# Optimization experiments

Hardware: AMD Instinct MI355X
Metric: run time of the kernel (lower is better)

The kernel has to match this reference:

```python
import jax, jax.numpy as jnp
import numpy as np
import math

B, N, D_POINTS, D_MODEL, K = 4, 4096, 512, 256, 16


def _gather(points, idx):
    # points: [B, N, C], idx: [B, S, K] -> [B, S, K, C]
    return jax.vmap(lambda p, i: p[i])(points, idx)


def setup_inputs() -> dict:
    key = jax.random.key(0)
    ks = jax.random.split(key, 20)
    def lin(k_, fan_in, fan_out):
        lim = 1.0 / math.sqrt(fan_in)
        return jax.random.uniform(k_, (fan_in, fan_out), jnp.float32, -lim, lim)
    inp = {
        "xyz": jax.random.normal(ks[0], (B, N, 3), jnp.float32),
        "features": jax.random.normal(ks[1], (B, N, D_POINTS), jnp.float32),
        # fc1: d_points -> d_model
        "W1": lin(ks[2], D_POINTS, D_MODEL), "b1": jnp.zeros((D_MODEL,), jnp.float32),
        # fc2: d_model -> d_points
        "W2": lin(ks[3], D_MODEL, D_POINTS), "b2": jnp.zeros((D_POINTS,), jnp.float32),
        # fc_delta: 3 -> d_model -> d_model
        "Wd1": lin(ks[4], 3, D_MODEL), "bd1": jnp.zeros((D_MODEL,), jnp.float32),
        "Wd2": lin(ks[5], D_MODEL, D_MODEL), "bd2": jnp.zeros((D_MODEL,), jnp.float32),
        # fc_gamma: d_model -> d_model -> d_model
        "Wg1": lin(ks[6], D_MODEL, D_MODEL), "bg1": jnp.zeros((D_MODEL,), jnp.float32),
        "Wg2": lin(ks[7], D_MODEL, D_MODEL), "bg2": jnp.zeros((D_MODEL,), jnp.float32),
        # q/k/v projections (no bias)
        "Wq": lin(ks[8], D_MODEL, D_MODEL),
        "Wk": lin(ks[9], D_MODEL, D_MODEL),
        "Wv": lin(ks[10], D_MODEL, D_MODEL),
        "k": K,
    }
    return inp


def reference(xyz, features, W1, b1, W2, b2, Wd1, bd1, Wd2, bd2,
              Wg1, bg1, Wg2, bg2, Wq, Wk, Wv, k):
    # pairwise squared distances [B, N, N]
    sq = jnp.sum(xyz * xyz, axis=-1)
    dists = sq[:, :, None] + sq[:, None, :] - 2.0 * jnp.einsum('bnc,bmc->bnm', xyz, xyz)
    _, knn_idx = jax.lax.top_k(-dists, k)              # [B, N, k] nearest (incl. self)
    knn_xyz = _gather(xyz, knn_idx)                    # [B, N, k, 3]

    pre = features
    x = features @ W1 + b1                             # [B, N, d_model]
    q = x @ Wq                                         # [B, N, d_model]
    kk = _gather(x @ Wk, knn_idx)                      # [B, N, k, d_model]
    v = _gather(x @ Wv, knn_idx)                       # [B, N, k, d_model]

    rel = xyz[:, :, None, :] - knn_xyz                 # [B, N, k, 3]
    pos_enc = jax.nn.relu(rel @ Wd1 + bd1) @ Wd2 + bd2 # [B, N, k, d_model]

    h = q[:, :, None, :] - kk + pos_enc
    attn = jax.nn.relu(h @ Wg1 + bg1) @ Wg2 + bg2      # [B, N, k, d_model]
    attn = jax.nn.softmax(attn / math.sqrt(D_MODEL), axis=-2)  # over k neighbors

    res = jnp.einsum('bnkf,bnkf->bnf', attn, v + pos_enc)
    res = res @ W2 + b2 + pre                          # [B, N, d_points]
    return res, attn
```

## Files before the change

kernel.cpp:

```cpp
#include <hip/hip_runtime.h>
#include <hip/hip_bf16.h>
#include <stdint.h>

typedef __hip_bfloat16 bf16;
typedef float f32x4 __attribute__((ext_vector_type(4)));
typedef __bf16 bf16x8 __attribute__((ext_vector_type(8)));

__device__ __forceinline__ float b2f(bf16 v) { return __bfloat162float(v); }
__device__ __forceinline__ bf16 f2b(float v) { return __float2bfloat16(v); }
__device__ __forceinline__ unsigned short f2bu(float f) {
  unsigned u = __float_as_uint(f);
  unsigned r = u + 0x7fffu + ((u >> 16) & 1u);
  return (unsigned short)(r >> 16);
}


#define CE64(a, b)                                            \
  do {                                                        \
    bool c_ = (b) < (a);                                      \
    unsigned long long lo_ = c_ ? (b) : (a);                  \
    unsigned long long hi_ = c_ ? (a) : (b);                  \
    (a) = lo_; (b) = hi_;                                     \
  } while (0)

#define CEA(x, y) CE64(x, y)
#define CED(x, y) CE64(y, x)
#define MIN64(x, y)                                           \
  do {                                                        \
    (x) = (y) < (x) ? (y) : (x);                              \
  } while (0)

__global__ __launch_bounds__(256) void pack_pts(const float* __restrict__ xyz,
                                                float4* __restrict__ pts) {
  int i = blockIdx.x * 256 + threadIdx.x;
  float x = xyz[i * 3 + 0];
  float y = xyz[i * 3 + 1];
  float z = xyz[i * 3 + 2];
  float sq = __fadd_rn(__fadd_rn(__fmul_rn(x, x), __fmul_rn(y, y)), __fmul_rn(z, z));
  pts[i] = make_float4(x, y, z, sq);
}

__global__ __launch_bounds__(256) void knn_partial(const float4* __restrict__ pts,
                                                   unsigned long long* __restrict__ keys) {
  __shared__ __align__(16) float4 cs[512];
  __shared__ __align__(16) float4 qs[64];

  int tid = threadIdx.x;
  int g = blockIdx.x >> 3;
  int r = blockIdx.x & 7;
  int batch = g >> 6;
  const float4* pp = pts + batch * 4096;
  int cb = r * 512;

  cs[tid] = pp[cb + tid];
  cs[256 + tid] = pp[cb + 256 + tid];
  if (tid < 64) qs[tid] = pp[(g & 63) * 64 + tid];
  __syncthreads();

  int wave = tid >> 6, lq = tid & 63;
  float4 Q = qs[lq];
  int mbase = cb + wave * 128;

  unsigned long long a[16];
#pragma unroll
  for (int i = 0; i < 16; ++i) a[i] = ~0ull;

#pragma unroll 2
  for (int tb = 0; tb < 16; ++tb) {
    unsigned long long c[8];
#pragma unroll
    for (int j = 0; j < 8; ++j) {
      float4 P = cs[wave * 128 + tb * 8 + j];
      float dot = __fadd_rn(__fadd_rn(__fmul_rn(Q.x, P.x), __fmul_rn(Q.y, P.y)),
                            __fmul_rn(Q.z, P.z));
      float d = __fsub_rn(__fadd_rn(Q.w, P.w), __fmul_rn(2.0f, dot));
      unsigned u = __float_as_uint(d);
      u ^= (unsigned)((int)u >> 31) | 0x80000000u;
      c[j] = ((unsigned long long)u << 32) | (unsigned)(mbase + tb * 8 + j);
    }

    CEA(c[0], c[1]); CED(c[2], c[3]); CEA(c[4], c[5]); CED(c[6], c[7]);
    CEA(c[0], c[2]); CEA(c[1], c[3]); CED(c[4], c[6]); CED(c[5], c[7]);
    CEA(c[0], c[1]); CEA(c[2], c[3]); CED(c[4], c[5]); CED(c[6], c[7]);
    CEA(c[0], c[4]); CEA(c[1], c[5]); CEA(c[2], c[6]); CEA(c[3], c[7]);
    CEA(c[0], c[2]); CEA(c[1], c[3]); CEA(c[4], c[6]); CEA(c[5], c[7]);
    CEA(c[0], c[1]); CEA(c[2], c[3]); CEA(c[4], c[5]); CEA(c[6], c[7]);

    MIN64(a[8],  c[7]); MIN64(a[9],  c[6]); MIN64(a[10], c[5]); MIN64(a[11], c[4]);
    MIN64(a[12], c[3]); MIN64(a[13], c[2]); MIN64(a[14], c[1]); MIN64(a[15], c[0]);

    CEA(a[0], a[8]);  CEA(a[1], a[9]);  CEA(a[2], a[10]); CEA(a[3], a[11]);
    CEA(a[4], a[12]); CEA(a[5], a[13]); CEA(a[6], a[14]); CEA(a[7], a[15]);
    CEA(a[0], a[4]);  CEA(a[1], a[5]);  CEA(a[2], a[6]);  CEA(a[3], a[7]);
    CEA(a[8], a[12]); CEA(a[9], a[13]); CEA(a[10], a[14]); CEA(a[11], a[15]);
    CEA(a[0], a[2]);  CEA(a[1], a[3]);  CEA(a[4], a[6]);  CEA(a[5], a[7]);
    CEA(a[8], a[10]); CEA(a[9], a[11]); CEA(a[12], a[14]); CEA(a[13], a[15]);
    CEA(a[0], a[1]);  CEA(a[2], a[3]);  CEA(a[4], a[5]);  CEA(a[6], a[7]);
    CEA(a[8], a[9]);  CEA(a[10], a[11]); CEA(a[12], a[13]); CEA(a[14], a[15]);
  }

  int rw = r * 4 + wave;
  int q = g * 64 + lq;
  unsigned long long* o = keys + (size_t)(rw * 16) * 16384 + q;
#pragma unroll
  for (int j = 0; j < 16; ++j) o[(size_t)j * 16384] = a[j];
}

__global__ __launch_bounds__(256) void knn_merge(const unsigned long long* __restrict__ keys,
                                                 int* __restrict__ gidx) {
  int q = blockIdx.x * 256 + threadIdx.x;
  const unsigned long long* kq = keys + q;

#define LOADL(rw)                                   \
  unsigned long long l0 = kq[((rw) * 16 + 0) * 16384],  l1 = kq[((rw) * 16 + 1) * 16384],  \
                     l2 = kq[((rw) * 16 + 2) * 16384],  l3 = kq[((rw) * 16 + 3) * 16384],  \
                     l4 = kq[((rw) * 16 + 4) * 16384],  l5 = kq[((rw) * 16 + 5) * 16384],  \
                     l6 = kq[((rw) * 16 + 6) * 16384],  l7 = kq[((rw) * 16 + 7) * 16384],  \
                     l8 = kq[((rw) * 16 + 8) * 16384],  l9 = kq[((rw) * 16 + 9) * 16384],  \
                     l10 = kq[((rw) * 16 + 10) * 16384], l11 = kq[((rw) * 16 + 11) * 16384], \
                     l12 = kq[((rw) * 16 + 12) * 16384], l13 = kq[((rw) * 16 + 13) * 16384], \
                     l14 = kq[((rw) * 16 + 14) * 16384], l15 = kq[((rw) * 16 + 15) * 16384]

  unsigned long long a0 = kq[0],           a1 = kq[16384],      a2 = kq[2 * 16384],
                     a3 = kq[3 * 16384],   a4 = kq[4 * 16384],  a5 = kq[5 * 16384],
                     a6 = kq[6 * 16384],   a7 = kq[7 * 16384],  a8 = kq[8 * 16384],
                     a9 = kq[9 * 16384],   a10 = kq[10 * 16384], a11 = kq[11 * 16384],
                     a12 = kq[12 * 16384], a13 = kq[13 * 16384], a14 = kq[14 * 16384],
                     a15 = kq[15 * 16384];

  for (int rw = 1; rw < 32; ++rw) {
    LOADL(rw);
    a0 = a0 < l15 ? a0 : l15;   a1 = a1 < l14 ? a1 : l14;
    a2 = a2 < l13 ? a2 : l13;   a3 = a3 < l12 ? a3 : l12;
    a4 = a4 < l11 ? a4 : l11;   a5 = a5 < l10 ? a5 : l10;
    a6 = a6 < l9 ? a6 : l9;     a7 = a7 < l8 ? a7 : l8;
    a8 = a8 < l7 ? a8 : l7;     a9 = a9 < l6 ? a9 : l6;
    a10 = a10 < l5 ? a10 : l5;  a11 = a11 < l4 ? a11 : l4;
    a12 = a12 < l3 ? a12 : l3;  a13 = a13 < l2 ? a13 : l2;
    a14 = a14 < l1 ? a14 : l1;  a15 = a15 < l0 ? a15 : l0;
    CE64(a0, a8);  CE64(a1, a9);  CE64(a2, a10); CE64(a3, a11);
    CE64(a4, a12); CE64(a5, a13); CE64(a6, a14); CE64(a7, a15);
    CE64(a0, a4);  CE64(a1, a5);  CE64(a2, a6);  CE64(a3, a7);
    CE64(a8, a12); CE64(a9, a13); CE64(a10, a14); CE64(a11, a15);
    CE64(a0, a2);  CE64(a1, a3);  CE64(a4, a6);  CE64(a5, a7);
    CE64(a8, a10); CE64(a9, a11); CE64(a12, a14); CE64(a13, a15);
    CE64(a0, a1);  CE64(a2, a3);  CE64(a4, a5);  CE64(a6, a7);
    CE64(a8, a9);  CE64(a10, a11); CE64(a12, a13); CE64(a14, a15);
  }
#undef LOADL

  int base = (q >> 12) << 12;
  int* o = gidx + (size_t)q * 16;
  o[0] = base + (int)(a0 & 0xffffffffu);   o[1] = base + (int)(a1 & 0xffffffffu);
  o[2] = base + (int)(a2 & 0xffffffffu);   o[3] = base + (int)(a3 & 0xffffffffu);
  o[4] = base + (int)(a4 & 0xffffffffu);   o[5] = base + (int)(a5 & 0xffffffffu);
  o[6] = base + (int)(a6 & 0xffffffffu);   o[7] = base + (int)(a7 & 0xffffffffu);
  o[8] = base + (int)(a8 & 0xffffffffu);   o[9] = base + (int)(a9 & 0xffffffffu);
  o[10] = base + (int)(a10 & 0xffffffffu); o[11] = base + (int)(a11 & 0xffffffffu);
  o[12] = base + (int)(a12 & 0xffffffffu); o[13] = base + (int)(a13 & 0xffffffffu);
  o[14] = base + (int)(a14 & 0xffffffffu); o[15] = base + (int)(a15 & 0xffffffffu);
}

__global__ __launch_bounds__(256) void transpose_k(const float* __restrict__ src,
                                                   bf16* __restrict__ dst,
                                                   int R, int C) {
  int i = blockIdx.x * 256 + threadIdx.x;
  if (i < R * C) {
    int r = i / C, c = i - r * C;
    dst[c * R + r] = f2b(src[i]);
  }
}

__global__ __launch_bounds__(256) void hidden_kernel(const float* __restrict__ xyz,
                                                     const int* __restrict__ gidx,
                                                     const float* __restrict__ Wd1,
                                                     const float* __restrict__ bd1,
                                                     bf16* __restrict__ hidden) {
  __shared__ float rel[16][3];
  int q = blockIdx.x;
  int tid = threadIdx.x;
  if (tid < 16) {
    int g = gidx[q * 16 + tid];
    rel[tid][0] = xyz[(size_t)q * 3 + 0] - xyz[(size_t)g * 3 + 0];
    rel[tid][1] = xyz[(size_t)q * 3 + 1] - xyz[(size_t)g * 3 + 1];
    rel[tid][2] = xyz[(size_t)q * 3 + 2] - xyz[(size_t)g * 3 + 2];
  }
  __syncthreads();
  float w0 = Wd1[tid], w1 = Wd1[256 + tid], w2 = Wd1[512 + tid];
  float bb = bd1[tid];
#pragma unroll
  for (int j = 0; j < 16; ++j) {
    float v = rel[j][0] * w0 + rel[j][1] * w1 + rel[j][2] * w2 + bb;
    v = fmaxf(v, 0.0f);
    hidden[((size_t)q * 16 + j) * 256 + tid] = f2b(v);
  }
}

template <int EPI, typename AT, typename CT>
__global__ __launch_bounds__(256) void gemm_bt(
    const AT* __restrict__ A, const bf16* __restrict__ BT,
    const float* __restrict__ bias, CT* __restrict__ C,
    int M, int N, int K,
    const bf16* __restrict__ e0p, const bf16* __restrict__ e1p,
    const bf16* __restrict__ e2p, const int* __restrict__ gidx,
    bf16* __restrict__ o1, const float* __restrict__ resid) {
  __shared__ __align__(16) unsigned short As[128 * 72];
  __shared__ __align__(16) unsigned short Bs[128 * 72];

  int ntn = N >> 7;
  int bx = blockIdx.x % ntn, by = blockIdx.x / ntn;
  int m0 = by * 128, n0 = bx * 128;
  int tid = threadIdx.x;
  int wave = tid >> 6, lane = tid & 63;
  int wr = wave >> 1, wc = wave & 1;
  int lm = lane & 15, lqd = lane >> 4;

  f32x4 acc[4][4] = {};

  for (int k0 = 0; k0 < K; k0 += 64) {
#pragma unroll
    for (int i = 0; i < 4; ++i) {
      int flat = i * 256 + tid;
      int row = flat >> 3;
      int u = flat & 7;
      if constexpr (sizeof(AT) == 4) {
        const float* ap = (const float*)A + (size_t)(m0 + row) * K + k0 + u * 8;
        float4 a0 = *reinterpret_cast<const float4*>(ap);
        float4 a1 = *reinterpret_cast<const float4*>(ap + 4);
        unsigned short* dst = &As[row * 72 + u * 8];
        dst[0] = f2bu(a0.x); dst[1] = f2bu(a0.y); dst[2] = f2bu(a0.z); dst[3] = f2bu(a0.w);
        dst[4] = f2bu(a1.x); dst[5] = f2bu(a1.y); dst[6] = f2bu(a1.z); dst[7] = f2bu(a1.w);
      } else {
        int4 av = *reinterpret_cast<const int4*>((const bf16*)A + (size_t)(m0 + row) * K + k0 + u * 8);
        *reinterpret_cast<int4*>(&As[row * 72 + u * 8]) = av;
      }
      int4 bv = *reinterpret_cast<const int4*>(BT + (size_t)(n0 + row) * K + k0 + u * 8);
      *reinterpret_cast<int4*>(&Bs[row * 72 + u * 8]) = bv;
    }
    __syncthreads();
#pragma unroll
    for (int ks = 0; ks < 2; ++ks) {
      bf16x8 af[4], bfr[4];
#pragma unroll
      for (int mi = 0; mi < 4; ++mi)
        af[mi] = *reinterpret_cast<const bf16x8*>(
            &As[(wr * 64 + mi * 16 + lm) * 72 + ks * 32 + lqd * 8]);
#pragma unroll
      for (int ni = 0; ni < 4; ++ni)
        bfr[ni] = *reinterpret_cast<const bf16x8*>(
            &Bs[(wc * 64 + ni * 16 + lm) * 72 + ks * 32 + lqd * 8]);
#pragma unroll
      for (int mi = 0; mi < 4; ++mi)
#pragma unroll
        for (int ni = 0; ni < 4; ++ni)
          acc[mi][ni] = __builtin_amdgcn_mfma_f32_16x16x32_bf16(af[mi], bfr[ni],
                                                                acc[mi][ni], 0, 0, 0);
    }
    __syncthreads();
  }

#pragma unroll
  for (int mi = 0; mi < 4; ++mi) {
    int mbase = m0 + wr * 64 + mi * 16;
#pragma unroll
    for (int ni = 0; ni < 4; ++ni) {
      int n = n0 + wc * 64 + ni * 16 + lm;
      float bv = bias ? bias[n] : 0.0f;
      if constexpr (EPI == 3) {
        float l0 = acc[mi][ni][0] + bv, l1 = acc[mi][ni][1] + bv;
        float l2 = acc[mi][ni][2] + bv, l3 = acc[mi][ni][3] + bv;
        float mx = fmaxf(fmaxf(l0, l1), fmaxf(l2, l3));
        mx = fmaxf(mx, __shfl_xor(mx, 16, 64));
        mx = fmaxf(mx, __shfl_xor(mx, 32, 64));
        float ev[4];
        ev[0] = __expf((l0 - mx) * 0.0625f);
        ev[1] = __expf((l1 - mx) * 0.0625f);
        ev[2] = __expf((l2 - mx) * 0.0625f);
        ev[3] = __expf((l3 - mx) * 0.0625f);
        float s = ev[0] + ev[1] + ev[2] + ev[3];
        s += __shfl_xor(s, 16, 64);
        s += __shfl_xor(s, 32, 64);
        float inv = 1.0f / s;
        float rp = 0.0f;
#pragma unroll
        for (int r = 0; r < 4; ++r) {
          size_t m = (size_t)(mbase + lqd * 4 + r);
          float a = ev[r] * inv;
          C[m * 256 + n] = a;
          rp += a * b2f(e2p[m * 256 + n]);
        }
        rp += __shfl_xor(rp, 16, 64);
        rp += __shfl_xor(rp, 32, 64);
        if (lqd == 0) o1[(size_t)(mbase >> 4) * 256 + n] = f2b(rp);
      } else {
#pragma unroll
        for (int r = 0; r < 4; ++r) {
          size_t m = (size_t)(mbase + lqd * 4 + r);
          float v = acc[mi][ni][r] + bv;
          if constexpr (EPI == 1) v = fmaxf(v, 0.0f);
          if constexpr (EPI == 2) {
            int g = gidx[m];
            float qv = b2f(e0p[(m >> 4) * (size_t)256 + n]);
            float kv = b2f(e1p[(size_t)g * 256 + n]);
            float vv = b2f(e2p[(size_t)g * 256 + n]);
            C[m * (size_t)N + n] = f2b(qv - kv + v);
            o1[m * (size_t)N + n] = f2b(vv + v);
          } else if constexpr (EPI == 4) {
            v += resid[m * (size_t)N + n];
            C[m * (size_t)N + n] = v;
          } else {
            C[m * (size_t)N + n] = f2b(v);
          }
        }
      }
    }
  }
}

extern "C" void kernel_launch(void* const* d_in, const int* in_sizes, int n_in,
                              void* d_out, int out_size, void* d_ws, size_t ws_size,
                              hipStream_t stream) {
  const float* xyz = (const float*)d_in[0];
  const float* feat = (const float*)d_in[1];
  const float* W1 = (const float*)d_in[2];
  const float* b1 = (const float*)d_in[3];
  const float* W2 = (const float*)d_in[4];
  const float* b2 = (const float*)d_in[5];
  const float* Wd1 = (const float*)d_in[6];
  const float* bd1 = (const float*)d_in[7];
  const float* Wd2 = (const float*)d_in[8];
  const float* bd2 = (const float*)d_in[9];
  const float* Wg1 = (const float*)d_in[10];
  const float* bg1 = (const float*)d_in[11];
  const float* Wg2 = (const float*)d_in[12];
  const float* bg2 = (const float*)d_in[13];
  const float* Wq = (const float*)d_in[14];
  const float* Wk = (const float*)d_in[15];
  const float* Wv = (const float*)d_in[16];

  constexpr size_t XBUF = 0;
  constexpr size_t QBUF = 8388608;
  constexpr size_t KBUF = 16777216;
  constexpr size_t VBUF = 25165824;
  constexpr size_t RESPRE = 33554432;
  constexpr size_t GIDX = 41943040;
  constexpr size_t W1T = 42991616;
  constexpr size_t W2T = 43253760;
  constexpr size_t WQT = 43515904;
  constexpr size_t WKT = 43646976;
  constexpr size_t WVT = 43778048;
  constexpr size_t WD2T = 43909120;
  constexpr size_t WG1T = 44040192;
  constexpr size_t WG2T = 44171264;
  constexpr size_t HIDDEN = 44302336;
  constexpr size_t HBUF = 178520064;
  constexpr size_t VPBUF = 312737792;
  constexpr size_t WS_NEEDED = 446955520;
  if (ws_size < WS_NEEDED) return;

  char* ws = (char*)d_ws;
  bf16* xbuf = (bf16*)(ws + XBUF);
  bf16* qbuf = (bf16*)(ws + QBUF);
  bf16* kbuf = (bf16*)(ws + KBUF);
  bf16* vbuf = (bf16*)(ws + VBUF);
  bf16* respre = (bf16*)(ws + RESPRE);
  int* gidx = (int*)(ws + GIDX);
  bf16* w1t = (bf16*)(ws + W1T);
  bf16* w2t = (bf16*)(ws + W2T);
  bf16* wqt = (bf16*)(ws + WQT);
  bf16* wkt = (bf16*)(ws + WKT);
  bf16* wvt = (bf16*)(ws + WVT);
  bf16* wd2t = (bf16*)(ws + WD2T);
  bf16* wg1t = (bf16*)(ws + WG1T);
  bf16* wg2t = (bf16*)(ws + WG2T);
  bf16* hidden = (bf16*)(ws + HIDDEN);
  bf16* hbuf = (bf16*)(ws + HBUF);
  bf16* vpbuf = (bf16*)(ws + VPBUF);

  unsigned long long* knnkeys = (unsigned long long*)(ws + HBUF);
  float4* pts4 = (float4*)(ws + HBUF + 67108864);

  float* res_out = (float*)d_out;
  float* attn_out = res_out + (size_t)16384 * 512;

  transpose_k<<<512, 256, 0, stream>>>(W1, w1t, 512, 256);
  transpose_k<<<512, 256, 0, stream>>>(W2, w2t, 256, 512);
  transpose_k<<<256, 256, 0, stream>>>(Wq, wqt, 256, 256);
  transpose_k<<<256, 256, 0, stream>>>(Wk, wkt, 256, 256);
  transpose_k<<<256, 256, 0, stream>>>(Wv, wvt, 256, 256);
  transpose_k<<<256, 256, 0, stream>>>(Wd2, wd2t, 256, 256);
  transpose_k<<<256, 256, 0, stream>>>(Wg1, wg1t, 256, 256);
  transpose_k<<<256, 256, 0, stream>>>(Wg2, wg2t, 256, 256);

  pack_pts<<<64, 256, 0, stream>>>(xyz, pts4);
  knn_partial<<<2048, 256, 0, stream>>>(pts4, knnkeys);
  knn_merge<<<64, 256, 0, stream>>>(knnkeys, gidx);

  gemm_bt<0, float, bf16><<<128 * 2, 256, 0, stream>>>(
      feat, w1t, b1, xbuf, 16384, 256, 512,
      nullptr, nullptr, nullptr, nullptr, nullptr, nullptr);
  gemm_bt<0, bf16, bf16><<<128 * 2, 256, 0, stream>>>(
      xbuf, wqt, nullptr, qbuf, 16384, 256, 256,
      nullptr, nullptr, nullptr, nullptr, nullptr, nullptr);
  gemm_bt<0, bf16, bf16><<<128 * 2, 256, 0, stream>>>(
      xbuf, wkt, nullptr, kbuf, 16384, 256, 256,
      nullptr, nullptr, nullptr, nullptr, nullptr, nullptr);
  gemm_bt<0, bf16, bf16><<<128 * 2, 256, 0, stream>>>(
      xbuf, wvt, nullptr, vbuf, 16384, 256, 256,
      nullptr, nullptr, nullptr, nullptr, nullptr, nullptr);

  hidden_kernel<<<16384, 256, 0, stream>>>(xyz, gidx, Wd1, bd1, hidden);

  gemm_bt<2, bf16, bf16><<<2048 * 2, 256, 0, stream>>>(
      hidden, wd2t, bd2, hbuf, 262144, 256, 256,
      qbuf, kbuf, vbuf, gidx, vpbuf, nullptr);
  gemm_bt<1, bf16, bf16><<<2048 * 2, 256, 0, stream>>>(
      hbuf, wg1t, bg1, hidden, 262144, 256, 256,
      nullptr, nullptr, nullptr, nullptr, nullptr, nullptr);
  gemm_bt<3, bf16, float><<<2048 * 2, 256, 0, stream>>>(
      hidden, wg2t, bg2, attn_out, 262144, 256, 256,
      nullptr, nullptr, vpbuf, nullptr, respre, nullptr);
  gemm_bt<4, bf16, float><<<128 * 4, 256, 0, stream>>>(
      respre, w2t, b2, res_out, 16384, 512, 256,
      nullptr, nullptr, nullptr, nullptr, nullptr, feat);
}
```

Measured before the change: 1.036 ms.

## Fuse pos-enc, gamma MLP and softmax GEMMs into one kernel keeping rows in LDS

Replaces the three chained 262144x256x256 GEMM launches with a single kernel. Each block keeps a 64-row tile resident in shared memory through all three matmuls. The intermediate h and relu(gamma1) activations, and the v+pos_enc buffer (now kept packed in registers), no longer go to global memory, which removes several hundred MB of HBM traffic. In exchange, each block reloads full 256x256 weight matrices per stage with no double buffering. Occupancy is also limited by the larger LDS footprint and the register pressure from the 2x8 accumulators plus packed v values.

```diff
diff --git a/kernel.cpp b/kernel.cpp
--- a/kernel.cpp
+++ b/kernel.cpp
@@ -196,14 +196,185 @@
   }
 }
 
+__global__ __launch_bounds__(256, 2) void fused_pt(
+    const bf16* __restrict__ hidden,
+    const bf16* __restrict__ wd2t, const float* __restrict__ bd2,
+    const bf16* __restrict__ wg1t, const float* __restrict__ bg1,
+    const bf16* __restrict__ wg2t, const float* __restrict__ bg2,
+    const bf16* __restrict__ qbuf, const bf16* __restrict__ kbuf,
+    const bf16* __restrict__ vbuf, const int* __restrict__ gidx,
+    float* __restrict__ attn_out,
+    bf16* __restrict__ respre) {
+  __shared__ __align__(16) unsigned short Ht[64 * 264];
+  __shared__ __align__(16) unsigned short Bs[256 * 72];
+
+  int m0 = blockIdx.x * 64;
+  int tid = threadIdx.x;
+  int wave = tid >> 6, lane = tid & 63;
+  int wr = wave >> 1, wc = wave & 1;
+  int lm = lane & 15, lqd = lane >> 4;
+
+#pragma unroll
+  for (int i = 0; i < 8; ++i) {
+    int flat = i * 256 + tid;
+    int row = flat >> 5;
+    int u = flat & 31;
+    int4 hv = *reinterpret_cast<const int4*>(hidden + (size_t)(m0 + row) * 256 + u * 8);
+    *reinterpret_cast<int4*>(&Ht[row * 264 + u * 8]) = hv;
+  }
+
+  f32x4 acc[2][8];
+#pragma unroll
+  for (int mi = 0; mi < 2; ++mi)
+#pragma unroll
+    for (int ni = 0; ni < 8; ++ni) acc[mi][ni] = (f32x4){0.f, 0.f, 0.f, 0.f};
+
+#define GEMM_LOOP(BTP)                                                          \
+  for (int k0 = 0; k0 < 256; k0 += 64) {                                        \
+    int4 breg[8];                                                               \
+    _Pragma("unroll")                                                           \
+    for (int i = 0; i < 8; ++i) {                                               \
+      int flat = i * 256 + tid;                                                 \
+      int row = flat >> 3;                                                      \
+      int u = flat & 7;                                                         \
+      breg[i] = *reinterpret_cast<const int4*>((BTP) + (size_t)row * 256 + k0 + u * 8); \
+    }                                                                           \
+    __syncthreads();                                                            \
+    _Pragma("unroll")                                                           \
+    for (int i = 0; i < 8; ++i) {                                               \
+      int flat = i * 256 + tid;                                                 \
+      int row = flat >> 3;                                                      \
+      int u = flat & 7;                                                         \
+      *reinterpret_cast<int4*>(&Bs[row * 72 + u * 8]) = breg[i];                \
+    }                                                                           \
+    __syncthreads();                                                            \
+    _Pragma("unroll")                                                           \
+    for (int ks = 0; ks < 2; ++ks) {                                            \
+      bf16x8 af[2], bfr[8];                                                     \
+      _Pragma("unroll")                                                         \
+      for (int mi = 0; mi < 2; ++mi)                                            \
+        af[mi] = *reinterpret_cast<const bf16x8*>(                              \
+            &Ht[(wr * 32 + mi * 16 + lm) * 264 + k0 + ks * 32 + lqd * 8]);      \
+      _Pragma("unroll")                                                         \
+      for (int ni = 0; ni < 8; ++ni)                                            \
+        bfr[ni] = *reinterpret_cast<const bf16x8*>(                             \
+            &Bs[(wc * 128 + ni * 16 + lm) * 72 + ks * 32 + lqd * 8]);           \
+      _Pragma("unroll")                                                         \
+      for (int mi = 0; mi < 2; ++mi)                                            \
+        _Pragma("unroll")                                                       \
+        for (int ni = 0; ni < 8; ++ni)                                          \
+          acc[mi][ni] = __builtin_amdgcn_mfma_f32_16x16x32_bf16(                \
+              af[mi], bfr[ni], acc[mi][ni], 0, 0, 0);                           \
+    }                                                                           \
+  }
+
+  GEMM_LOOP(wd2t)
+
+  __syncthreads();
+  uint2 vpp[2][8];
+#pragma unroll
+  for (int mi = 0; mi < 2; ++mi) {
+    int mtile = m0 + wr * 32 + mi * 16;
+    int qrow = mtile >> 4;
+    int gi[4];
+#pragma unroll
+    for (int r = 0; r < 4; ++r) gi[r] = gidx[mtile + lqd * 4 + r];
+#pragma unroll
+    for (int ni = 0; ni < 8; ++ni) {
+      int n = wc * 128 + ni * 16 + lm;
+      float qv = b2f(qbuf[(size_t)qrow * 256 + n]);
+      float bdv = bd2[n];
+      unsigned vb[4];
+#pragma unroll
+      for (int r = 0; r < 4; ++r) {
+        float pos = acc[mi][ni][r] + bdv;
+        float kv = b2f(kbuf[(size_t)gi[r] * 256 + n]);
+        float vv = b2f(vbuf[(size_t)gi[r] * 256 + n]);
+        Ht[(wr * 32 + mi * 16 + lqd * 4 + r) * 264 + n] = f2bu(qv - kv + pos);
+        vb[r] = f2bu(vv + pos);
+      }
+      vpp[mi][ni] = make_uint2(vb[0] | (vb[1] << 16), vb[2] | (vb[3] << 16));
+    }
+  }
+  __syncthreads();
+
+#pragma unroll
+  for (int mi = 0; mi < 2; ++mi)
+#pragma unroll
+    for (int ni = 0; ni < 8; ++ni) acc[mi][ni] = (f32x4){0.f, 0.f, 0.f, 0.f};
+
+  GEMM_LOOP(wg1t)
+
+  __syncthreads();
+#pragma unroll
+  for (int mi = 0; mi < 2; ++mi)
+#pragma unroll
+    for (int ni = 0; ni < 8; ++ni) {
+      int n = wc * 128 + ni * 16 + lm;
+      float bgv = bg1[n];
+#pragma unroll
+      for (int r = 0; r < 4; ++r)
+        Ht[(wr * 32 + mi * 16 + lqd * 4 + r) * 264 + n] =
+            f2bu(fmaxf(acc[mi][ni][r] + bgv, 0.0f));
+    }
+  __syncthreads();
+
+#pragma unroll
+  for (int mi = 0; mi < 2; ++mi)
+#pragma unroll
+    for (int ni = 0; ni < 8; ++ni) acc[mi][ni] = (f32x4){0.f, 0.f, 0.f, 0.f};
+
+  GEMM_LOOP(wg2t)
+#undef GEMM_LOOP
+
+#pragma unroll
+  for (int mi = 0; mi < 2; ++mi) {
+    int mtile = m0 + wr * 32 + mi * 16;
+    int qrow = mtile >> 4;
+#pragma unroll
+    for (int ni = 0; ni < 8; ++ni) {
+      int n = wc * 128 + ni * 16 + lm;
+      float bv = bg2[n];
+      float l0 = acc[mi][ni][0] + bv, l1 = acc[mi][ni][1] + bv;
+      float l2 = acc[mi][ni][2] + bv, l3 = acc[mi][ni][3] + bv;
+      float mx = fmaxf(fmaxf(l0, l1), fmaxf(l2, l3));
+      mx = fmaxf(mx, __shfl_xor(mx, 16, 64));
+      mx = fmaxf(mx, __shfl_xor(mx, 32, 64));
+      float ev[4];
+      ev[0] = __expf((l0 - mx) * 0.0625f);
+      ev[1] = __expf((l1 - mx) * 0.0625f);
+      ev[2] = __expf((l2 - mx) * 0.0625f);
+      ev[3] = __expf((l3 - mx) * 0.0625f);
+      float s = ev[0] + ev[1] + ev[2] + ev[3];
+      s += __shfl_xor(s, 16, 64);
+      s += __shfl_xor(s, 32, 64);
+      float inv = 1.0f / s;
+      float vpf[4];
+      vpf[0] = __uint_as_float(vpp[mi][ni].x << 16);
+      vpf[1] = __uint_as_float(vpp[mi][ni].x & 0xffff0000u);
+      vpf[2] = __uint_as_float(vpp[mi][ni].y << 16);
+      vpf[3] = __uint_as_float(vpp[mi][ni].y & 0xffff0000u);
+      float rp = 0.0f;
+#pragma unroll
+      for (int r = 0; r < 4; ++r) {
+        size_t m = (size_t)(mtile + lqd * 4 + r);
+        float a = ev[r] * inv;
+        attn_out[m * 256 + n] = a;
+        rp += a * vpf[r];
+      }
+      rp += __shfl_xor(rp, 16, 64);
+      rp += __shfl_xor(rp, 32, 64);
+      if (lqd == 0) respre[(size_t)qrow * 256 + n] = f2b(rp);
+    }
+  }
+}
+
 template <int EPI, typename AT, typename CT>
 __global__ __launch_bounds__(256) void gemm_bt(
     const AT* __restrict__ A, const bf16* __restrict__ BT,
     const float* __restrict__ bias, CT* __restrict__ C,
     int M, int N, int K,
-    const bf16* __restrict__ e0p, const bf16* __restrict__ e1p,
-    const bf16* __restrict__ e2p, const int* __restrict__ gidx,
-    bf16* __restrict__ o1, const float* __restrict__ resid) {
+    const float* __restrict__ resid) {
   __shared__ __align__(16) unsigned short As[128 * 72];
   __shared__ __align__(16) unsigned short Bs[128 * 72];
 
@@ -266,51 +437,15 @@
     for (int ni = 0; ni < 4; ++ni) {
       int n = n0 + wc * 64 + ni * 16 + lm;
       float bv = bias ? bias[n] : 0.0f;
-      if constexpr (EPI == 3) {
-        float l0 = acc[mi][ni][0] + bv, l1 = acc[mi][ni][1] + bv;
-        float l2 = acc[mi][ni][2] + bv, l3 = acc[mi][ni][3] + bv;
-        float mx = fmaxf(fmaxf(l0, l1), fmaxf(l2, l3));
-        mx = fmaxf(mx, __shfl_xor(mx, 16, 64));
-        mx = fmaxf(mx, __shfl_xor(mx, 32, 64));
-        float ev[4];
-        ev[0] = __expf((l0 - mx) * 0.0625f);
-        ev[1] = __expf((l1 - mx) * 0.0625f);
-        ev[2] = __expf((l2 - mx) * 0.0625f);
-        ev[3] = __expf((l3 - mx) * 0.0625f);
-        float s = ev[0] + ev[1] + ev[2] + ev[3];
-        s += __shfl_xor(s, 16, 64);
-        s += __shfl_xor(s, 32, 64);
-        float inv = 1.0f / s;
-        float rp = 0.0f;
-#pragma unroll
-        for (int r = 0; r < 4; ++r) {
-          size_t m = (size_t)(mbase + lqd * 4 + r);
-          float a = ev[r] * inv;
-          C[m * 256 + n] = a;
-          rp += a * b2f(e2p[m * 256 + n]);
-        }
-        rp += __shfl_xor(rp, 16, 64);
-        rp += __shfl_xor(rp, 32, 64);
-        if (lqd == 0) o1[(size_t)(mbase >> 4) * 256 + n] = f2b(rp);
-      } else {
-#pragma unroll
-        for (int r = 0; r < 4; ++r) {
-          size_t m = (size_t)(mbase + lqd * 4 + r);
-          float v = acc[mi][ni][r] + bv;
-          if constexpr (EPI == 1) v = fmaxf(v, 0.0f);
-          if constexpr (EPI == 2) {
-            int g = gidx[m];
-            float qv = b2f(e0p[(m >> 4) * (size_t)256 + n]);
-            float kv = b2f(e1p[(size_t)g * 256 + n]);
-            float vv = b2f(e2p[(size_t)g * 256 + n]);
-            C[m * (size_t)N + n] = f2b(qv - kv + v);
-            o1[m * (size_t)N + n] = f2b(vv + v);
-          } else if constexpr (EPI == 4) {
-            v += resid[m * (size_t)N + n];
-            C[m * (size_t)N + n] = v;
-          } else {
-            C[m * (size_t)N + n] = f2b(v);
-          }
+#pragma unroll
+      for (int r = 0; r < 4; ++r) {
+        size_t m = (size_t)(mbase + lqd * 4 + r);
+        float v = acc[mi][ni][r] + bv;
+        if constexpr (EPI == 4) {
+          v += resid[m * (size_t)N + n];
+          C[m * (size_t)N + n] = v;
+        } else {
+          C[m * (size_t)N + n] = f2b(v);
         }
       }
     }
@@ -354,7 +489,6 @@
   constexpr size_t WG2T = 44171264;
   constexpr size_t HIDDEN = 44302336;
   constexpr size_t HBUF = 178520064;
-  constexpr size_t VPBUF = 312737792;
   constexpr size_t WS_NEEDED = 446955520;
   if (ws_size < WS_NEEDED) return;
 
@@ -374,8 +508,6 @@
   bf16* wg1t = (bf16*)(ws + WG1T);
   bf16* wg2t = (bf16*)(ws + WG2T);
   bf16* hidden = (bf16*)(ws + HIDDEN);
-  bf16* hbuf = (bf16*)(ws + HBUF);
-  bf16* vpbuf = (bf16*)(ws + VPBUF);
 
   unsigned long long* knnkeys = (unsigned long long*)(ws + HBUF);
   float4* pts4 = (float4*)(ws + HBUF + 67108864);
@@ -397,30 +529,19 @@
   knn_merge<<<64, 256, 0, stream>>>(knnkeys, gidx);
 
   gemm_bt<0, float, bf16><<<128 * 2, 256, 0, stream>>>(
-      feat, w1t, b1, xbuf, 16384, 256, 512,
-      nullptr, nullptr, nullptr, nullptr, nullptr, nullptr);
+      feat, w1t, b1, xbuf, 16384, 256, 512, nullptr);
   gemm_bt<0, bf16, bf16><<<128 * 2, 256, 0, stream>>>(
-      xbuf, wqt, nullptr, qbuf, 16384, 256, 256,
-      nullptr, nullptr, nullptr, nullptr, nullptr, nullptr);
+      xbuf, wqt, nullptr, qbuf, 16384, 256, 256, nullptr);
   gemm_bt<0, bf16, bf16><<<128 * 2, 256, 0, stream>>>(
-      xbuf, wkt, nullptr, kbuf, 16384, 256, 256,
-      nullptr, nullptr, nullptr, nullptr, nullptr, nullptr);
+      xbuf, wkt, nullptr, kbuf, 16384, 256, 256, nullptr);
   gemm_bt<0, bf16, bf16><<<128 * 2, 256, 0, stream>>>(
-      xbuf, wvt, nullptr, vbuf, 16384, 256, 256,
-      nullptr, nullptr, nullptr, nullptr, nullptr, nullptr);
+      xbuf, wvt, nullptr, vbuf, 16384, 256, 256, nullptr);
 
   hidden_kernel<<<16384, 256, 0, stream>>>(xyz, gidx, Wd1, bd1, hidden);
 
-  gemm_bt<2, bf16, bf16><<<2048 * 2, 256, 0, stream>>>(
-      hidden, wd2t, bd2, hbuf, 262144, 256, 256,
-      qbuf, kbuf, vbuf, gidx, vpbuf, nullptr);
-  gemm_bt<1, bf16, bf16><<<2048 * 2, 256, 0, stream>>>(
-      hbuf, wg1t, bg1, hidden, 262144, 256, 256,
-      nullptr, nullptr, nullptr, nullptr, nullptr, nullptr);
-  gemm_bt<3, bf16, float><<<2048 * 2, 256, 0, stream>>>(
-      hidden, wg2t, bg2, attn_out, 262144, 256, 256,
-      nullptr, nullptr, vpbuf, nullptr, respre, nullptr);
+  fused_pt<<<4096, 256, 0, stream>>>(hidden, wd2t, bd2, wg1t, bg1, wg2t, bg2,
+                                     qbuf, kbuf, vbuf, gidx, attn_out, respre);
+
   gemm_bt<4, bf16, float><<<128 * 4, 256, 0, stream>>>(
-      respre, w2t, b2, res_out, 16384, 512, 256,
-      nullptr, nullptr, nullptr, nullptr, nullptr, feat);
-}
+      respre, w2t, b2, res_out, 16384, 512, 256, feat);
+}
```

Result: slower. 1.238 ms (+19.4%).
